# Optimization experiments

Hardware: AMD Instinct MI355X
Metric: run time of the kernel (lower is better)

Reference implementation:

```python
import jax, jax.numpy as jnp
import numpy as np


def setup_inputs() -> dict:
    key = jax.random.key(0)
    ks = jax.random.split(key, 7)
    B, D, N, R = 256, 5120, 16, 160  # batch, d_inner, d_state, dt_rank
    x = jax.random.normal(ks[0], (B, D), jnp.float32)
    h0 = jax.random.normal(ks[1], (B, D, N), jnp.float32)
    W_x_dt = jax.random.normal(ks[2], (D, R), jnp.float32) * (1.0 / np.sqrt(D))
    W_dt = jax.random.normal(ks[3], (R, D), jnp.float32) * (1.0 / np.sqrt(R))
    b_dt = jax.random.normal(ks[4], (D,), jnp.float32)
    W_BC = jax.random.normal(ks[5], (D, 2 * N), jnp.float32) * (1.0 / np.sqrt(D))
    A_log = jax.random.normal(ks[6], (D, N), jnp.float32)
    return {"x": x, "h0": h0, "W_x_dt": W_x_dt, "W_dt": W_dt,
            "b_dt": b_dt, "W_BC": W_BC, "A_log": A_log}


def reference(x, h0, W_x_dt, W_dt, b_dt, W_BC, A_log):
    # Single-token Mamba selective SSM step (batch dims squeezed: x [B,D], h0 [B,D,N]).
    N = A_log.shape[1]
    # delta_t = softplus(dt_proj(delta_t_proj(x)))  -> [B, D]
    dt = jax.nn.softplus((x @ W_x_dt) @ W_dt + b_dt)
    # BC projection, split into B and C parts -> [B, N] each
    BC = x @ W_BC
    Bm, Cm = BC[:, :N], BC[:, N:]
    A = -jnp.exp(A_log)                              # [D, N]
    delta_A = jnp.exp(A[None, :, :] * dt[:, :, None])   # [B, D, N]
    delta_Bx = (dt * x)[:, :, None] * Bm[:, None, :]     # [B, D, N]
    h = delta_A * h0 + delta_Bx                          # new hidden state
    # y = h @ C (per-batch bmm over state dim) + x residual
    y = jnp.einsum('bdn,bn->bd', h, Cm) + x              # [B, D]
    return y
```

## Files before the change

### kernel.cpp

```cpp
#include <hip/hip_runtime.h>
#include <math.h>

#define BB 256
#define DD 5120
#define NN 16
#define RR 160
#define CT 192
#define NSPLIT 32
#define TMP_ELEMS (BB * CT)
#define NEGA_ELEMS (DD * NN)

__global__ __launch_bounds__(256) void k1_gemm(const float* __restrict__ x,
                                               const float* __restrict__ Wxdt,
                                               const float* __restrict__ Wbc,
                                               float* __restrict__ part) {
    __shared__ float xs[32][68];
    __shared__ float ws[32][64];
    const int tid = threadIdx.x;
    const int tx = tid & 15, ty = tid >> 4;
    const int c0 = blockIdx.x * 64;
    const int b0 = blockIdx.y * 64;
    const int k0 = blockIdx.z * 160;
    float acc[4][4] = {};

    for (int kc = 0; kc < 160; kc += 32) {
        {
            const int i  = tid >> 3;
            const int j4 = (tid & 7) * 4;
            #pragma unroll
            for (int rep = 0; rep < 2; ++rep) {
                const int row = i + rep * 32;
                const float4 v = *(const float4*)&x[(size_t)(b0 + row) * DD + k0 + kc + j4];
                xs[j4 + 0][row] = v.x;
                xs[j4 + 1][row] = v.y;
                xs[j4 + 2][row] = v.z;
                xs[j4 + 3][row] = v.w;
            }
        }
        {
            const int c4 = (tid & 15) * 4;
            const int r0 = tid >> 4;
            #pragma unroll
            for (int rep = 0; rep < 2; ++rep) {
                const int r  = r0 + rep * 16;
                const int kg = k0 + kc + r;
                const int cg = c0 + c4;
                float4 v;
                if (cg < RR) v = *(const float4*)&Wxdt[(size_t)kg * RR + cg];
                else         v = *(const float4*)&Wbc[(size_t)kg * 32 + (cg - RR)];
                *(float4*)&ws[r][c4] = v;
            }
        }
        __syncthreads();
        #pragma unroll
        for (int k = 0; k < 32; ++k) {
            const float4 a4 = *(const float4*)&xs[k][ty * 4];
            const float4 w4 = *(const float4*)&ws[k][tx * 4];
            const float av[4] = {a4.x, a4.y, a4.z, a4.w};
            const float wv[4] = {w4.x, w4.y, w4.z, w4.w};
            #pragma unroll
            for (int u = 0; u < 4; ++u)
                #pragma unroll
                for (int v = 0; v < 4; ++v)
                    acc[u][v] = fmaf(av[u], wv[v], acc[u][v]);
        }
        __syncthreads();
    }

    float* p = part + (size_t)blockIdx.z * TMP_ELEMS;
    #pragma unroll
    for (int u = 0; u < 4; ++u) {
        const int b = b0 + ty * 4 + u;
        *(float4*)&p[b * CT + c0 + tx * 4] =
            make_float4(acc[u][0], acc[u][1], acc[u][2], acc[u][3]);
    }
}

__global__ __launch_bounds__(256) void k_red(const float* __restrict__ part,
                                             const float* __restrict__ Alog,
                                             float* __restrict__ tmp,
                                             float* __restrict__ negA) {
    const int idx = blockIdx.x * 256 + threadIdx.x;
    if (idx < TMP_ELEMS) {
        float s = 0.f;
        #pragma unroll
        for (int z = 0; z < NSPLIT; ++z) s += part[(size_t)z * TMP_ELEMS + idx];
        tmp[idx] = s;
    } else {
        const int j = idx - TMP_ELEMS;
        negA[j] = -__expf(Alog[j]);
    }
}

__global__ __launch_bounds__(256) void k23_fused(const float* __restrict__ x,
                                                 const float* __restrict__ h0,
                                                 const float* __restrict__ Wdt,
                                                 const float* __restrict__ bdt,
                                                 const float* __restrict__ tmp,
                                                 const float* __restrict__ negA,
                                                 float* __restrict__ out) {
    __shared__ float ts[32][34];
    __shared__ float ws[32][64];
    __shared__ float As[64][17];
    __shared__ float BCs[32][33];
    const int tid = threadIdx.x;
    const int tx = tid & 15, ty = tid >> 4;
    const int d0 = blockIdx.x * 64;
    const int b0 = blockIdx.y * 32;

    {
        const int i  = tid >> 2;
        const int n4 = (tid & 3) * 4;
        const float4 v = *(const float4*)&negA[(size_t)(d0 + i) * NN + n4];
        As[i][n4 + 0] = v.x; As[i][n4 + 1] = v.y;
        As[i][n4 + 2] = v.z; As[i][n4 + 3] = v.w;
    }
    {
        const int row = tid >> 3;
        const int c4  = (tid & 7) * 4;
        const float4 v = *(const float4*)&tmp[(size_t)(b0 + row) * CT + RR + c4];
        BCs[row][c4 + 0] = v.x; BCs[row][c4 + 1] = v.y;
        BCs[row][c4 + 2] = v.z; BCs[row][c4 + 3] = v.w;
    }

    float acc[2][4] = {};
    for (int kc = 0; kc < RR; kc += 32) {
        {
            const int row = tid >> 3;
            const int j4  = (tid & 7) * 4;
            const float4 v = *(const float4*)&tmp[(size_t)(b0 + row) * CT + kc + j4];
            ts[j4 + 0][row] = v.x;
            ts[j4 + 1][row] = v.y;
            ts[j4 + 2][row] = v.z;
            ts[j4 + 3][row] = v.w;
        }
        {
            const int c4 = (tid & 15) * 4;
            const int r0 = tid >> 4;
            #pragma unroll
            for (int rep = 0; rep < 2; ++rep) {
                const int r = r0 + rep * 16;
                *(float4*)&ws[r][c4] = *(const float4*)&Wdt[(size_t)(kc + r) * DD + d0 + c4];
            }
        }
        __syncthreads();
        #pragma unroll
        for (int k = 0; k < 32; ++k) {
            const float a0 = ts[k][ty * 2 + 0];
            const float a1 = ts[k][ty * 2 + 1];
            const float4 w4 = *(const float4*)&ws[k][tx * 4];
            const float wv[4] = {w4.x, w4.y, w4.z, w4.w};
            #pragma unroll
            for (int v = 0; v < 4; ++v) {
                acc[0][v] = fmaf(a0, wv[v], acc[0][v]);
                acc[1][v] = fmaf(a1, wv[v], acc[1][v]);
            }
        }
        __syncthreads();
    }

    const float4 bv = *(const float4*)&bdt[d0 + tx * 4];
    const float bb[4] = {bv.x, bv.y, bv.z, bv.w};

    #pragma unroll
    for (int u = 0; u < 2; ++u) {
        const int b = b0 + ty * 2 + u;
        const size_t base = (size_t)b * DD + d0 + tx * 4;
        const float4 xv = *(const float4*)&x[base];
        const float xs4[4] = {xv.x, xv.y, xv.z, xv.w};
        const float* bm = &BCs[ty * 2 + u][0];
        const float* cm = &BCs[ty * 2 + u][16];
        float y[4];
        #pragma unroll
        for (int v = 0; v < 4; ++v) {
            const int dsub = tx * 4 + v;
            const float z  = acc[u][v] + bb[v];
            const float dt = fmaxf(z, 0.f) + log1pf(__expf(-fabsf(z)));
            const float xe = xs4[v];
            const float dtx = dt * xe;
            const float* hp = &h0[(base + (size_t)v) * NN];
            float acc_y = xe;
            #pragma unroll
            for (int n4 = 0; n4 < NN; n4 += 4) {
                const float4 a4 = *(const float4*)&As[dsub][n4];
                const float4 h4 = *(const float4*)&hp[n4];
                const float av[4] = {a4.x, a4.y, a4.z, a4.w};
                const float hv[4] = {h4.x, h4.y, h4.z, h4.w};
                #pragma unroll
                for (int q = 0; q < 4; ++q) {
                    const int n = n4 + q;
                    const float dA = __expf(av[q] * dt);
                    const float h  = fmaf(dA, hv[q], dtx * bm[n]);
                    acc_y = fmaf(h, cm[n], acc_y);
                }
            }
            y[v] = acc_y;
        }
        *(float4*)&out[base] = make_float4(y[0], y[1], y[2], y[3]);
    }
}

extern "C" void kernel_launch(void* const* d_in, const int* in_sizes, int n_in,
                              void* d_out, int out_size, void* d_ws, size_t ws_size,
                              hipStream_t stream) {
    const float* x    = (const float*)d_in[0];
    const float* h0   = (const float*)d_in[1];
    const float* Wxdt = (const float*)d_in[2];
    const float* Wdt  = (const float*)d_in[3];
    const float* bdt  = (const float*)d_in[4];
    const float* Wbc  = (const float*)d_in[5];
    const float* Alog = (const float*)d_in[6];
    float* out = (float*)d_out;

    float* part = (float*)d_ws;
    float* tmp  = part + (size_t)NSPLIT * TMP_ELEMS;
    float* negA = tmp + TMP_ELEMS;

    k1_gemm<<<dim3(3, 4, NSPLIT), 256, 0, stream>>>(x, Wxdt, Wbc, part);
    k_red<<<dim3((TMP_ELEMS + NEGA_ELEMS) / 256), 256, 0, stream>>>(part, Alog, tmp, negA);
    k23_fused<<<dim3(DD / 64, BB / 32), 256, 0, stream>>>(x, h0, Wdt, bdt, tmp, negA, out);
}
```

Measured before the change: 185.7 us.

## Restructure fused SSM kernel per-thread d-pairs, inline negA, double K-split

Doubles the K-split of the first GEMM to 64 slices of 80, giving more blocks. Computes -exp(A_log) inside the fused kernel's registers, so the reduction kernel no longer writes negA and the fused kernel no longer reads it back. Rewrites the fused kernel so each thread owns two adjacent d columns across 4 batch rows, reading W_dt straight from global memory in a register-accumulated loop instead of LDS tiles. The trade-offs are that W_dt is re-read by 64 batch-row blocks, the partial-sum buffer doubles in size, and register pressure rises.

```diff
diff --git a/kernel.cpp b/kernel.cpp
--- a/kernel.cpp
+++ b/kernel.cpp
@@ -6,54 +6,46 @@
 #define NN 16
 #define RR 160
 #define CT 192
-#define NSPLIT 32
+#define NSPLIT 64
+#define KSPL 80
 #define TMP_ELEMS (BB * CT)
-#define NEGA_ELEMS (DD * NN)
 
 __global__ __launch_bounds__(256) void k1_gemm(const float* __restrict__ x,
                                                const float* __restrict__ Wxdt,
                                                const float* __restrict__ Wbc,
                                                float* __restrict__ part) {
-    __shared__ float xs[32][68];
-    __shared__ float ws[32][64];
+    __shared__ float xs[16][68];
+    __shared__ float ws[16][64];
     const int tid = threadIdx.x;
     const int tx = tid & 15, ty = tid >> 4;
     const int c0 = blockIdx.x * 64;
     const int b0 = blockIdx.y * 64;
-    const int k0 = blockIdx.z * 160;
+    const int k0 = blockIdx.z * KSPL;
     float acc[4][4] = {};
 
-    for (int kc = 0; kc < 160; kc += 32) {
+    for (int kc = 0; kc < KSPL; kc += 16) {
         {
-            const int i  = tid >> 3;
-            const int j4 = (tid & 7) * 4;
-            #pragma unroll
-            for (int rep = 0; rep < 2; ++rep) {
-                const int row = i + rep * 32;
-                const float4 v = *(const float4*)&x[(size_t)(b0 + row) * DD + k0 + kc + j4];
-                xs[j4 + 0][row] = v.x;
-                xs[j4 + 1][row] = v.y;
-                xs[j4 + 2][row] = v.z;
-                xs[j4 + 3][row] = v.w;
-            }
+            const int row = tid >> 2;
+            const int j4  = (tid & 3) * 4;
+            const float4 v = *(const float4*)&x[(size_t)(b0 + row) * DD + k0 + kc + j4];
+            xs[j4 + 0][row] = v.x;
+            xs[j4 + 1][row] = v.y;
+            xs[j4 + 2][row] = v.z;
+            xs[j4 + 3][row] = v.w;
         }
         {
+            const int r  = tid >> 4;
             const int c4 = (tid & 15) * 4;
-            const int r0 = tid >> 4;
-            #pragma unroll
-            for (int rep = 0; rep < 2; ++rep) {
-                const int r  = r0 + rep * 16;
-                const int kg = k0 + kc + r;
-                const int cg = c0 + c4;
-                float4 v;
-                if (cg < RR) v = *(const float4*)&Wxdt[(size_t)kg * RR + cg];
-                else         v = *(const float4*)&Wbc[(size_t)kg * 32 + (cg - RR)];
-                *(float4*)&ws[r][c4] = v;
-            }
+            const int kg = k0 + kc + r;
+            const int cg = c0 + c4;
+            float4 v;
+            if (cg < RR) v = *(const float4*)&Wxdt[(size_t)kg * RR + cg];
+            else         v = *(const float4*)&Wbc[(size_t)kg * 32 + (cg - RR)];
+            *(float4*)&ws[r][c4] = v;
         }
         __syncthreads();
         #pragma unroll
-        for (int k = 0; k < 32; ++k) {
+        for (int k = 0; k < 16; ++k) {
             const float4 a4 = *(const float4*)&xs[k][ty * 4];
             const float4 w4 = *(const float4*)&ws[k][tx * 4];
             const float av[4] = {a4.x, a4.y, a4.z, a4.w};
@@ -77,126 +69,118 @@
 }
 
 __global__ __launch_bounds__(256) void k_red(const float* __restrict__ part,
-                                             const float* __restrict__ Alog,
-                                             float* __restrict__ tmp,
-                                             float* __restrict__ negA) {
+                                             float* __restrict__ tmp) {
     const int idx = blockIdx.x * 256 + threadIdx.x;
-    if (idx < TMP_ELEMS) {
-        float s = 0.f;
-        #pragma unroll
-        for (int z = 0; z < NSPLIT; ++z) s += part[(size_t)z * TMP_ELEMS + idx];
-        tmp[idx] = s;
-    } else {
-        const int j = idx - TMP_ELEMS;
-        negA[j] = -__expf(Alog[j]);
-    }
+    float s = 0.f;
+    #pragma unroll
+    for (int z = 0; z < NSPLIT; ++z) s += part[(size_t)z * TMP_ELEMS + idx];
+    tmp[idx] = s;
 }
 
 __global__ __launch_bounds__(256) void k23_fused(const float* __restrict__ x,
                                                  const float* __restrict__ h0,
                                                  const float* __restrict__ Wdt,
                                                  const float* __restrict__ bdt,
+                                                 const float* __restrict__ Alog,
                                                  const float* __restrict__ tmp,
-                                                 const float* __restrict__ negA,
                                                  float* __restrict__ out) {
-    __shared__ float ts[32][34];
-    __shared__ float ws[32][64];
-    __shared__ float As[64][17];
-    __shared__ float BCs[32][33];
+    __shared__ float4 ts4[RR];
+    __shared__ float  BCs[4][32];
     const int tid = threadIdx.x;
-    const int tx = tid & 15, ty = tid >> 4;
-    const int d0 = blockIdx.x * 64;
-    const int b0 = blockIdx.y * 32;
-
-    {
-        const int i  = tid >> 2;
-        const int n4 = (tid & 3) * 4;
-        const float4 v = *(const float4*)&negA[(size_t)(d0 + i) * NN + n4];
-        As[i][n4 + 0] = v.x; As[i][n4 + 1] = v.y;
-        As[i][n4 + 2] = v.z; As[i][n4 + 3] = v.w;
-    }
-    {
-        const int row = tid >> 3;
-        const int c4  = (tid & 7) * 4;
-        const float4 v = *(const float4*)&tmp[(size_t)(b0 + row) * CT + RR + c4];
-        BCs[row][c4 + 0] = v.x; BCs[row][c4 + 1] = v.y;
-        BCs[row][c4 + 2] = v.z; BCs[row][c4 + 3] = v.w;
-    }
-
-    float acc[2][4] = {};
-    for (int kc = 0; kc < RR; kc += 32) {
-        {
-            const int row = tid >> 3;
-            const int j4  = (tid & 7) * 4;
-            const float4 v = *(const float4*)&tmp[(size_t)(b0 + row) * CT + kc + j4];
-            ts[j4 + 0][row] = v.x;
-            ts[j4 + 1][row] = v.y;
-            ts[j4 + 2][row] = v.z;
-            ts[j4 + 3][row] = v.w;
-        }
-        {
-            const int c4 = (tid & 15) * 4;
-            const int r0 = tid >> 4;
+    const int d0  = blockIdx.x * 512;
+    const int b0  = blockIdx.y * 4;
+    const int d2  = d0 + tid * 2;
+
+    if (tid < RR) {
+        float4 t;
+        t.x = tmp[(size_t)(b0 + 0) * CT + tid];
+        t.y = tmp[(size_t)(b0 + 1) * CT + tid];
+        t.z = tmp[(size_t)(b0 + 2) * CT + tid];
+        t.w = tmp[(size_t)(b0 + 3) * CT + tid];
+        ts4[tid] = t;
+    } else if (tid < RR + 32) {
+        const int idx = tid - RR;
+        const int j  = idx >> 3;
+        const int c4 = (idx & 7) * 4;
+        const float4 v = *(const float4*)&tmp[(size_t)(b0 + j) * CT + RR + c4];
+        BCs[j][c4 + 0] = v.x; BCs[j][c4 + 1] = v.y;
+        BCs[j][c4 + 2] = v.z; BCs[j][c4 + 3] = v.w;
+    }
+
+    float na0[NN], na1[NN];
+    #pragma unroll
+    for (int q4 = 0; q4 < 4; ++q4) {
+        const float4 a = *(const float4*)&Alog[(size_t)d2 * NN + q4 * 4];
+        na0[q4 * 4 + 0] = -__expf(a.x); na0[q4 * 4 + 1] = -__expf(a.y);
+        na0[q4 * 4 + 2] = -__expf(a.z); na0[q4 * 4 + 3] = -__expf(a.w);
+        const float4 c = *(const float4*)&Alog[(size_t)(d2 + 1) * NN + q4 * 4];
+        na1[q4 * 4 + 0] = -__expf(c.x); na1[q4 * 4 + 1] = -__expf(c.y);
+        na1[q4 * 4 + 2] = -__expf(c.z); na1[q4 * 4 + 3] = -__expf(c.w);
+    }
+    __syncthreads();
+
+    float acc[4][2] = {};
+    #pragma unroll 8
+    for (int r = 0; r < RR; ++r) {
+        const float2 w = *(const float2*)&Wdt[(size_t)r * DD + d2];
+        const float4 tv = ts4[r];
+        acc[0][0] = fmaf(tv.x, w.x, acc[0][0]); acc[0][1] = fmaf(tv.x, w.y, acc[0][1]);
+        acc[1][0] = fmaf(tv.y, w.x, acc[1][0]); acc[1][1] = fmaf(tv.y, w.y, acc[1][1]);
+        acc[2][0] = fmaf(tv.z, w.x, acc[2][0]); acc[2][1] = fmaf(tv.z, w.y, acc[2][1]);
+        acc[3][0] = fmaf(tv.w, w.x, acc[3][0]); acc[3][1] = fmaf(tv.w, w.y, acc[3][1]);
+    }
+
+    const float2 bb = *(const float2*)&bdt[d2];
+
+    #pragma unroll
+    for (int j = 0; j < 4; ++j) {
+        const int b = b0 + j;
+        const size_t base = (size_t)b * DD + d2;
+
+        const float z0  = acc[j][0] + bb.x;
+        const float dt0 = fmaxf(z0, 0.f) + log1pf(__expf(-fabsf(z0)));
+        const float z1  = acc[j][1] + bb.y;
+        const float dt1 = fmaxf(z1, 0.f) + log1pf(__expf(-fabsf(z1)));
+
+        const float2 xe = *(const float2*)&x[base];
+        const float dtx0 = dt0 * xe.x;
+        const float dtx1 = dt1 * xe.y;
+
+        const float* hp = &h0[base * NN];
+        float4 ha[4], hb[4];
+        #pragma unroll
+        for (int i = 0; i < 4; ++i) ha[i] = *(const float4*)&hp[i * 4];
+        #pragma unroll
+        for (int i = 0; i < 4; ++i) hb[i] = *(const float4*)&hp[NN + i * 4];
+
+        float bm[NN], cm[NN];
+        #pragma unroll
+        for (int q4 = 0; q4 < 4; ++q4) {
+            const float4 v = *(const float4*)&BCs[j][q4 * 4];
+            bm[q4 * 4 + 0] = v.x; bm[q4 * 4 + 1] = v.y;
+            bm[q4 * 4 + 2] = v.z; bm[q4 * 4 + 3] = v.w;
+            const float4 w = *(const float4*)&BCs[j][16 + q4 * 4];
+            cm[q4 * 4 + 0] = w.x; cm[q4 * 4 + 1] = w.y;
+            cm[q4 * 4 + 2] = w.z; cm[q4 * 4 + 3] = w.w;
+        }
+
+        float y0a = xe.x, y0b = 0.f, y1a = xe.y, y1b = 0.f;
+        #pragma unroll
+        for (int q4 = 0; q4 < 4; ++q4) {
+            const float hv0[4] = {ha[q4].x, ha[q4].y, ha[q4].z, ha[q4].w};
+            const float hv1[4] = {hb[q4].x, hb[q4].y, hb[q4].z, hb[q4].w};
             #pragma unroll
-            for (int rep = 0; rep < 2; ++rep) {
-                const int r = r0 + rep * 16;
-                *(float4*)&ws[r][c4] = *(const float4*)&Wdt[(size_t)(kc + r) * DD + d0 + c4];
+            for (int q = 0; q < 4; ++q) {
+                const int n = q4 * 4 + q;
+                const float dA0 = __expf(na0[n] * dt0);
+                const float h00 = fmaf(dA0, hv0[q], dtx0 * bm[n]);
+                const float dA1 = __expf(na1[n] * dt1);
+                const float h11 = fmaf(dA1, hv1[q], dtx1 * bm[n]);
+                if (n & 1) { y0b = fmaf(h00, cm[n], y0b); y1b = fmaf(h11, cm[n], y1b); }
+                else       { y0a = fmaf(h00, cm[n], y0a); y1a = fmaf(h11, cm[n], y1a); }
             }
         }
-        __syncthreads();
-        #pragma unroll
-        for (int k = 0; k < 32; ++k) {
-            const float a0 = ts[k][ty * 2 + 0];
-            const float a1 = ts[k][ty * 2 + 1];
-            const float4 w4 = *(const float4*)&ws[k][tx * 4];
-            const float wv[4] = {w4.x, w4.y, w4.z, w4.w};
-            #pragma unroll
-            for (int v = 0; v < 4; ++v) {
-                acc[0][v] = fmaf(a0, wv[v], acc[0][v]);
-                acc[1][v] = fmaf(a1, wv[v], acc[1][v]);
-            }
-        }
-        __syncthreads();
-    }
-
-    const float4 bv = *(const float4*)&bdt[d0 + tx * 4];
-    const float bb[4] = {bv.x, bv.y, bv.z, bv.w};
-
-    #pragma unroll
-    for (int u = 0; u < 2; ++u) {
-        const int b = b0 + ty * 2 + u;
-        const size_t base = (size_t)b * DD + d0 + tx * 4;
-        const float4 xv = *(const float4*)&x[base];
-        const float xs4[4] = {xv.x, xv.y, xv.z, xv.w};
-        const float* bm = &BCs[ty * 2 + u][0];
-        const float* cm = &BCs[ty * 2 + u][16];
-        float y[4];
-        #pragma unroll
-        for (int v = 0; v < 4; ++v) {
-            const int dsub = tx * 4 + v;
-            const float z  = acc[u][v] + bb[v];
-            const float dt = fmaxf(z, 0.f) + log1pf(__expf(-fabsf(z)));
-            const float xe = xs4[v];
-            const float dtx = dt * xe;
-            const float* hp = &h0[(base + (size_t)v) * NN];
-            float acc_y = xe;
-            #pragma unroll
-            for (int n4 = 0; n4 < NN; n4 += 4) {
-                const float4 a4 = *(const float4*)&As[dsub][n4];
-                const float4 h4 = *(const float4*)&hp[n4];
-                const float av[4] = {a4.x, a4.y, a4.z, a4.w};
-                const float hv[4] = {h4.x, h4.y, h4.z, h4.w};
-                #pragma unroll
-                for (int q = 0; q < 4; ++q) {
-                    const int n = n4 + q;
-                    const float dA = __expf(av[q] * dt);
-                    const float h  = fmaf(dA, hv[q], dtx * bm[n]);
-                    acc_y = fmaf(h, cm[n], acc_y);
-                }
-            }
-            y[v] = acc_y;
-        }
-        *(float4*)&out[base] = make_float4(y[0], y[1], y[2], y[3]);
+        *(float2*)&out[base] = make_float2(y0a + y0b, y1a + y1b);
     }
 }
 
@@ -214,9 +198,8 @@
 
     float* part = (float*)d_ws;
     float* tmp  = part + (size_t)NSPLIT * TMP_ELEMS;
-    float* negA = tmp + TMP_ELEMS;
 
     k1_gemm<<<dim3(3, 4, NSPLIT), 256, 0, stream>>>(x, Wxdt, Wbc, part);
-    k_red<<<dim3((TMP_ELEMS + NEGA_ELEMS) / 256), 256, 0, stream>>>(part, Alog, tmp, negA);
-    k23_fused<<<dim3(DD / 64, BB / 32), 256, 0, stream>>>(x, h0, Wdt, bdt, tmp, negA, out);
-}
+    k_red<<<dim3(TMP_ELEMS / 256), 256, 0, stream>>>(part, tmp);
+    k23_fused<<<dim3(10, 64), 256, 0, stream>>>(x, h0, Wdt, bdt, Alog, tmp, out);
+}
```

Result: slower. 191.0 us (+2.8%).
